# Optimization experiments

Hardware: AMD Instinct MI355X
Metric: run time of the kernel (lower is better)

Reference implementation:

```python
import jax, jax.numpy as jnp
import numpy as np

B, S, D_IN, E, H = 4, 2048, 768, 768, 12
HD = E // H                      # 64
WIN_PCT = 10                     # window_size init arg (percent of valid length)
MAX_LEN = 2048
MIN_WIN = 2
PAD = -1e9
TEMP = 1.0


def setup_inputs() -> dict:
    key = jax.random.key(0)
    k1, k2, k3 = jax.random.split(key, 3)
    return {
        "x": jax.random.normal(k1, (B, S, D_IN), dtype=jnp.float32),
        "src_key_padding_mask": jnp.zeros((B, S), dtype=jnp.int32),   # 0 = valid token
        "matrix_mask": jnp.zeros((B, S, S), dtype=jnp.float32),       # additive mask, 0 or PAD
        "qkv_w": jax.random.normal(k2, (3 * E, D_IN), dtype=jnp.float32) * 0.02,
        "qkv_b": jnp.zeros((3 * E,), dtype=jnp.float32),
        "o_w": jax.random.normal(k3, (E, E), dtype=jnp.float32) * 0.02,
        "o_b": jnp.zeros((E,), dtype=jnp.float32),
    }


def _sliding_window_mask(src_key_padding_mask, matrix_mask):
    # per-sample window size = ceil(valid_len * WIN_PCT / 100), clamped to >= MIN_WIN
    lens = (src_key_padding_mask == 0).sum(axis=1)                    # [B]
    clipped = jnp.minimum(lens, MAX_LEN).astype(jnp.float32)
    wsz = jnp.maximum(jnp.ceil(clipped * WIN_PCT / 100.0), MIN_WIN)   # [B] float ok for compare
    idx = jnp.arange(S)
    dist = jnp.abs(idx[None, :, None] - idx[None, None, :])           # [1,S,S]
    window_mask = dist > wsz[:, None, None]                           # [B,S,S] bool
    merged = window_mask | (matrix_mask == PAD)
    return jnp.where(merged, PAD, matrix_mask)                        # [B,S,S]


def reference(x, src_key_padding_mask, matrix_mask, qkv_w, qkv_b, o_w, o_b):
    mask = _sliding_window_mask(src_key_padding_mask, matrix_mask)    # [B,S,S]
    qkv = x @ qkv_w.T + qkv_b                                         # [B,S,3E]
    # torch: reshape(B,S,H,3*HD) then chunk along last dim
    qkv = qkv.reshape(B, S, H, 3 * HD).transpose(0, 2, 1, 3)          # [B,H,S,3*HD]
    q, k, v = jnp.split(qkv, 3, axis=-1)                              # each [B,H,S,HD]
    scale = 1.0 / np.sqrt(HD)
    logits = jnp.einsum("bhqd,bhkd->bhqk", q, k) * scale + mask[:, None]
    attn = jax.nn.softmax(logits / TEMP, axis=-1)                     # [B,H,S,S]
    values = jnp.einsum("bhqk,bhkd->bhqd", attn, v)                   # [B,H,S,HD]
    attn_mean = attn.mean(axis=1)                                     # [B,S,S]
    values = values.transpose(0, 2, 1, 3).reshape(B, S, E)            # [B,S,E]
    o = values @ o_w.T + o_b
    return (o, attn_mean)
```

## Files before the change

kernel.cpp:

```cpp
#include <hip/hip_runtime.h>

#define SEQ 2048
#define NB 4
#define DIN 768
#define EDIM 768
#define NH 12
#define QKVN 2304
#define QKW 1536
#define SCALE 0.125f
#define PADV -1e9f
#define INV12 (0.0833333333f)
#define PSW 520

typedef unsigned short ushort_t;
typedef __attribute__((ext_vector_type(8))) short bf16x8;
typedef __attribute__((ext_vector_type(4))) float f32x4;

__device__ __forceinline__ float bf2f(ushort_t u) {
    union { unsigned int i; float f; } v; v.i = ((unsigned int)u) << 16; return v.f;
}
__device__ __forceinline__ ushort_t f2bf(float f) {
    union { float f; unsigned int i; } v; v.f = f;
    unsigned int r = (v.i + 0x7fffu + ((v.i >> 16) & 1u)) >> 16;
    return (ushort_t)r;
}
__device__ __forceinline__ void gl_lds16(const ushort_t* g, ushort_t* l) {
    __builtin_amdgcn_global_load_lds(
        (const __attribute__((address_space(1))) unsigned int*)(g),
        (__attribute__((address_space(3))) unsigned int*)(l),
        16, 0, 0);
}

__global__ void wsz_kernel(const int* __restrict__ mask, int* __restrict__ wszp) {
    int b = blockIdx.x;
    __shared__ int cnt;
    if (threadIdx.x == 0) cnt = 0;
    __syncthreads();
    int local = 0;
    for (int s = threadIdx.x; s < SEQ; s += blockDim.x)
        local += (mask[b * SEQ + s] == 0) ? 1 : 0;
    for (int o = 32; o; o >>= 1) local += __shfl_down(local, o, 64);
    if ((threadIdx.x & 63) == 0) atomicAdd(&cnt, local);
    __syncthreads();
    if (threadIdx.x == 0) {
        int len = cnt; if (len > 2048) len = 2048;
        float w = ceilf(((float)len * 10.0f) / 100.0f);
        int wsz = (int)w;
        if (wsz < 2) wsz = 2;
        wszp[b] = wsz;
    }
}

__global__ void cvt_kernel(const float* __restrict__ in, ushort_t* __restrict__ out, int n4) {
    int i = blockIdx.x * blockDim.x + threadIdx.x;
    if (i < n4) {
        float4 f = ((const float4*)in)[i];
        ushort4 u;
        u.x = f2bf(f.x); u.y = f2bf(f.y); u.z = f2bf(f.z); u.w = f2bf(f.w);
        ((ushort4*)out)[i] = u;
    }
}

__global__ void flag_kernel(const float* __restrict__ mmask, const int* __restrict__ wszp,
                            int* __restrict__ flags) {
    const int b = blockIdx.z, i16 = blockIdx.y;
    const int wsz = wszp[b];
    const int i0 = i16 * 16;
    const int jt0 = max(0, i0 - wsz) >> 6;
    const int jt1 = min(SEQ - 1, i0 + 15 + wsz) >> 6;
    const int jt = jt0 + blockIdx.x;
    if (jt > jt1) return;
    int any = 0;
    for (int e = threadIdx.x; e < 1024; e += 256) {
        int row = e >> 6, col = e & 63;
        float v = mmask[((size_t)b * SEQ + i0 + row) * SEQ + jt * 64 + col];
        any |= (v != 0.f);
    }
    if (any) flags[(b * 128 + i16) * 32 + jt] = 1;
}

template<int MODE>
__global__ __launch_bounds__(256) void mfma_gemm128(
    const ushort_t* __restrict__ A, const ushort_t* __restrict__ Bw,
    const float* __restrict__ bias, float* __restrict__ outf,
    ushort_t* __restrict__ qk, ushort_t* __restrict__ vt, int N, int K)
{
    __shared__ __align__(16) ushort_t Al[128 * 64];
    __shared__ __align__(16) ushort_t Bl[128 * 64];
    const int tid  = threadIdx.x;
    const int w    = tid >> 6;
    const int l    = tid & 63;
    const int quad = l >> 4;
    const int lr   = l & 15;
    const int mw   = (w >> 1) * 64;
    const int nw   = (w & 1) * 64;
    const int bm   = blockIdx.y * 128;
    const int bn   = blockIdx.x * 128;
    const int srow = l >> 3;
    const int sg   = (l & 7) ^ srow;

    f32x4 acc[4][4];
    #pragma unroll
    for (int i = 0; i < 4; ++i)
        #pragma unroll
        for (int j = 0; j < 4; ++j)
            #pragma unroll
            for (int r = 0; r < 4; ++r) acc[i][j][r] = 0.f;

    const ushort_t* ga = A  + (size_t)(bm + w * 32 + srow) * K + sg * 8;
    const ushort_t* gb = Bw + (size_t)(bn + w * 32 + srow) * K + sg * 8;
    ushort_t* la = &Al[(w * 32) * 64];
    ushort_t* lb = &Bl[(w * 32) * 64];

    for (int k0 = 0; k0 < K; k0 += 64) {
        __syncthreads();
        #pragma unroll
        for (int i = 0; i < 4; ++i)
            gl_lds16(ga + (size_t)(i * 8) * K + k0, la + i * 8 * 64);
        #pragma unroll
        for (int i = 0; i < 4; ++i)
            gl_lds16(gb + (size_t)(i * 8) * K + k0, lb + i * 8 * 64);
        __syncthreads();
        #pragma unroll
        for (int s = 0; s < 2; ++s) {
            bf16x8 af[4], bf[4];
            #pragma unroll
            for (int t = 0; t < 4; ++t)
                af[t] = *(const bf16x8*)&Al[(mw + t * 16 + lr) * 64 + (((4 * s + quad) ^ (lr & 7)) * 8)];
            #pragma unroll
            for (int t = 0; t < 4; ++t)
                bf[t] = *(const bf16x8*)&Bl[(nw + t * 16 + lr) * 64 + (((4 * s + quad) ^ (lr & 7)) * 8)];
            #pragma unroll
            for (int mt = 0; mt < 4; ++mt)
                #pragma unroll
                for (int nt = 0; nt < 4; ++nt)
                    acc[mt][nt] = __builtin_amdgcn_mfma_f32_16x16x32_bf16(af[mt], bf[nt], acc[mt][nt], 0, 0, 0);
        }
    }

    #pragma unroll
    for (int nt = 0; nt < 4; ++nt) {
        const int gn = bn + nw + nt * 16 + lr;
        const float bv = bias[gn];
        const int hh  = gn / 192;
        const int rem = gn - hh * 192;
        #pragma unroll
        for (int mt = 0; mt < 4; ++mt) {
            const int gm0 = bm + mw + mt * 16 + quad * 4;
            if (MODE == 0) {
                #pragma unroll
                for (int r = 0; r < 4; ++r)
                    outf[(size_t)(gm0 + r) * N + gn] = acc[mt][nt][r] + bv;
            } else if (rem < 128) {
                #pragma unroll
                for (int r = 0; r < 4; ++r)
                    qk[(size_t)(gm0 + r) * QKW + hh * 128 + rem] = f2bf(acc[mt][nt][r] + bv);
            } else {
                const int bb  = gm0 >> 11;
                const int tok = gm0 & (SEQ - 1);
                ushort4 st;
                st.x = f2bf(acc[mt][nt][0] + bv);
                st.y = f2bf(acc[mt][nt][1] + bv);
                st.z = f2bf(acc[mt][nt][2] + bv);
                st.w = f2bf(acc[mt][nt][3] + bv);
                *(ushort4*)&vt[((size_t)(bb * NH + hh) * 64 + (rem - 128)) * SEQ + tok] = st;
            }
        }
    }
}

__global__ __launch_bounds__(512) void attn_kernel(
    const ushort_t* __restrict__ qk,
    const ushort_t* __restrict__ vt,
    const float* __restrict__ mmask,
    const int* __restrict__ wszp,
    const int* __restrict__ flags,
    ushort_t* __restrict__ values,
    float* __restrict__ attn_out)
{
    __shared__ __align__(16) ushort_t Ps[2][16 * PSW];
    __shared__ float lsump[2][4][16];
    const int tid  = threadIdx.x;
    const int w    = tid >> 6;
    const int hg   = w >> 2;
    const int ww   = w & 3;
    const int lane = tid & 63;
    const int quad = lane >> 4;
    const int lr   = lane & 15;

    const int lin  = blockIdx.x;
    const int s    = lin & 1;
    const int b    = (lin >> 1) & 3;
    const int i16  = (lin >> 3) + 64 * s;
    const int iq0  = i16 * 16;

    const int wsz  = wszp[b];
    const int jlo  = max(0, iq0 - wsz);
    const int jhi  = min(SEQ - 1, iq0 + 15 + wsz);
    const int jt0  = jlo >> 6;
    const int nch  = (jhi >> 6) - jt0 + 1;
    const int jbase = jt0 << 6;
    const int span  = nch << 6;
    const int fbase = (b * 128 + i16) * 32;

    const int arow = tid & 15;
    const int acg  = tid >> 4;
    float acc[16];
    #pragma unroll
    for (int k = 0; k < 16; ++k) acc[k] = 0.f;

    const ushort_t* kbase = qk + (size_t)b * SEQ * QKW + 64;
    const ushort_t* vhead = vt + (size_t)b * NH * 64 * SEQ;

    for (int hp = 0; hp < NH / 2; ++hp) {
        const int h  = hp * 2 + hg;
        const int hq = h * 128;
        const ushort_t* qbase = qk + (size_t)(b * SEQ + iq0 + lr) * QKW + hq;
        const bf16x8 qf0 = *(const bf16x8*)(qbase + quad * 8);
        const bf16x8 qf1 = *(const bf16x8*)(qbase + 32 + quad * 8);

        float ls[4] = {0.f, 0.f, 0.f, 0.f};
        #pragma unroll
        for (int cc = 0; cc < 2; ++cc) {
            const int ci = ww + cc * 4;
            if (ci < nch) {
                const int jc = jbase + ci * 64;
                f32x4 s4[4];
                #pragma unroll
                for (int t = 0; t < 4; ++t) {
                    const ushort_t* kr = kbase + (size_t)(jc + t * 16 + lr) * QKW + hq;
                    bf16x8 kf0 = *(const bf16x8*)(kr + quad * 8);
                    bf16x8 kf1 = *(const bf16x8*)(kr + 32 + quad * 8);
                    #pragma unroll
                    for (int r = 0; r < 4; ++r) s4[t][r] = 0.f;
                    s4[t] = __builtin_amdgcn_mfma_f32_16x16x32_bf16(qf0, kf0, s4[t], 0, 0, 0);
                    s4[t] = __builtin_amdgcn_mfma_f32_16x16x32_bf16(qf1, kf1, s4[t], 0, 0, 0);
                }
                const int anym = flags[fbase + jt0 + ci];
                #pragma unroll
                for (int t = 0; t < 4; ++t) {
                    const int gj = jc + t * 16 + lr;
                    #pragma unroll
                    for (int r = 0; r < 4; ++r) {
                        const int gi = iq0 + quad * 4 + r;
                        float mm = 0.f;
                        if (anym) mm = mmask[((size_t)b * SEQ + gi) * SEQ + gj];
                        const int dist = gi > gj ? gi - gj : gj - gi;
                        const float p = (dist > wsz) ? 0.f : __expf(fmaf(s4[t][r], SCALE, mm));
                        ls[r] += p;
                        Ps[hg][(quad * 4 + r) * PSW + (ci * 64 + t * 16 + lr)] = f2bf(p);
                    }
                }
            }
        }
        #pragma unroll
        for (int r = 0; r < 4; ++r) {
            #pragma unroll
            for (int m = 8; m; m >>= 1) ls[r] += __shfl_xor(ls[r], m, 16);
        }
        if (lr == 0) {
            #pragma unroll
            for (int r = 0; r < 4; ++r) lsump[hg][ww][quad * 4 + r] = ls[r];
        }
        __syncthreads();

        if (acg * 16 < span) {
            const float l0 = lsump[0][0][arow] + lsump[0][1][arow] + lsump[0][2][arow] + lsump[0][3][arow];
            const float l1 = lsump[1][0][arow] + lsump[1][1][arow] + lsump[1][2][arow] + lsump[1][3][arow];
            const float sc0 = INV12 / l0;
            const float sc1 = INV12 / l1;
            const ushort_t* p0 = &Ps[0][arow * PSW + acg * 16];
            const ushort_t* p1 = &Ps[1][arow * PSW + acg * 16];
            #pragma unroll
            for (int k = 0; k < 4; ++k) {
                ushort4 u0 = *(const ushort4*)(p0 + k * 4);
                ushort4 u1 = *(const ushort4*)(p1 + k * 4);
                acc[k * 4 + 0] = fmaf(bf2f(u0.x), sc0, fmaf(bf2f(u1.x), sc1, acc[k * 4 + 0]));
                acc[k * 4 + 1] = fmaf(bf2f(u0.y), sc0, fmaf(bf2f(u1.y), sc1, acc[k * 4 + 1]));
                acc[k * 4 + 2] = fmaf(bf2f(u0.z), sc0, fmaf(bf2f(u1.z), sc1, acc[k * 4 + 2]));
                acc[k * 4 + 3] = fmaf(bf2f(u0.w), sc0, fmaf(bf2f(u1.w), sc1, acc[k * 4 + 3]));
            }
        }

        {
            f32x4 oacc;
            #pragma unroll
            for (int r = 0; r < 4; ++r) oacc[r] = 0.f;
            const ushort_t* vrow = vhead + (size_t)(hq / 2 + ww * 16 + lr) * SEQ + jbase;
            for (int ci = 0; ci < nch; ++ci) {
                const int tok0 = ci * 64;
                #pragma unroll
                for (int s2 = 0; s2 < 2; ++s2) {
                    bf16x8 pa = *(const bf16x8*)&Ps[hg][lr * PSW + tok0 + s2 * 32 + quad * 8];
                    bf16x8 vf = *(const bf16x8*)(vrow + tok0 + s2 * 32 + quad * 8);
                    oacc = __builtin_amdgcn_mfma_f32_16x16x32_bf16(pa, vf, oacc, 0, 0, 0);
                }
            }
            float lr4[4];
            #pragma unroll
            for (int r = 0; r < 4; ++r)
                lr4[r] = lsump[hg][0][quad * 4 + r] + lsump[hg][1][quad * 4 + r] +
                         lsump[hg][2][quad * 4 + r] + lsump[hg][3][quad * 4 + r];
            #pragma unroll
            for (int r = 0; r < 4; ++r) {
                const int row = iq0 + quad * 4 + r;
                values[(size_t)(b * SEQ + row) * EDIM + h * 64 + ww * 16 + lr] =
                    f2bf(oacc[r] / lr4[r]);
            }
        }
        __syncthreads();
    }

    if (acg * 16 < span) {
        float* dst = attn_out + ((size_t)b * SEQ + iq0 + arow) * SEQ + jbase + acg * 16;
        #pragma unroll
        for (int k = 0; k < 4; ++k) {
            float4 v = { acc[k * 4 + 0], acc[k * 4 + 1], acc[k * 4 + 2], acc[k * 4 + 3] };
            *(float4*)(dst + k * 4) = v;
        }
    }
    {
        const int c4lo = jbase >> 2;
        const int c4hi = (jbase + span) >> 2;
        const float4 z = {0.f, 0.f, 0.f, 0.f};
        for (int f = tid; f < 16 * 512; f += 512) {
            const int i  = f >> 9;
            const int c4 = f & 511;
            if (c4 < c4lo || c4 >= c4hi)
                *(float4*)(attn_out + ((size_t)b * SEQ + iq0 + i) * SEQ + c4 * 4) = z;
        }
    }
}

extern "C" void kernel_launch(void* const* d_in, const int* in_sizes, int n_in,
                              void* d_out, int out_size, void* d_ws, size_t ws_size,
                              hipStream_t stream) {
    const float* x      = (const float*)d_in[0];
    const int*   pad    = (const int*)d_in[1];
    const float* mmask  = (const float*)d_in[2];
    const float* qkv_w  = (const float*)d_in[3];
    const float* qkv_b  = (const float*)d_in[4];
    const float* o_w    = (const float*)d_in[5];
    const float* o_b    = (const float*)d_in[6];

    float* out_o    = (float*)d_out;
    float* out_attn = out_o + (size_t)NB * SEQ * EDIM;

    ushort_t* qk     = (ushort_t*)d_ws;
    ushort_t* vt     = qk + (size_t)NB * SEQ * QKW;
    ushort_t* xb     = vt + (size_t)NB * NH * 64 * SEQ;
    ushort_t* values = xb;
    ushort_t* wqkvb  = xb + (size_t)NB * SEQ * DIN;
    ushort_t* wob    = wqkvb + (size_t)QKVN * DIN;
    int*      wszp   = (int*)(wob + (size_t)EDIM * EDIM);
    int*      flags  = wszp + 4;

    hipMemsetAsync(flags, 0, (size_t)NB * 128 * 32 * sizeof(int), stream);

    wsz_kernel<<<NB, 256, 0, stream>>>(pad, wszp);
    flag_kernel<<<dim3(8, 128, NB), 256, 0, stream>>>(mmask, wszp, flags);

    const int nx = NB * SEQ * DIN / 4, nw1 = QKVN * DIN / 4, nw2 = EDIM * EDIM / 4;
    cvt_kernel<<<(nx  + 255) / 256, 256, 0, stream>>>(x,     xb,    nx);
    cvt_kernel<<<(nw1 + 255) / 256, 256, 0, stream>>>(qkv_w, wqkvb, nw1);
    cvt_kernel<<<(nw2 + 255) / 256, 256, 0, stream>>>(o_w,   wob,   nw2);

    mfma_gemm128<1><<<dim3(QKVN / 128, (NB * SEQ) / 128), 256, 0, stream>>>(
        xb, wqkvb, qkv_b, nullptr, qk, vt, QKVN, DIN);

    attn_kernel<<<512, 512, 0, stream>>>(
        qk, vt, mmask, wszp, flags, values, out_attn);

    mfma_gemm128<0><<<dim3(EDIM / 128, (NB * SEQ) / 128), 256, 0, stream>>>(
        values, wob, o_b, out_o, nullptr, nullptr, EDIM, EDIM);
}
```

Baseline: 345.1 us.

## Halve attention query tile to 8 rows, double blocks; merge convert kernels

The attention kernel now processes 8 query rows per block instead of 16 and launches 1024 blocks instead of 512. The 16-row MFMA tiles are filled by duplicating the 8 query rows, and only the valid half is stored. This raises block-level parallelism and shrinks the key span each block covers, at the cost of half-wasted MFMA work and duplicated K/V loads. The three fp32-to-bf16 convert launches are also merged into a single kernel to cut launch overhead.

```diff
diff --git a/kernel.cpp b/kernel.cpp
--- a/kernel.cpp
+++ b/kernel.cpp
@@ -11,6 +11,7 @@
 #define PADV -1e9f
 #define INV12 (0.0833333333f)
 #define PSW 520
+#define TQR 8
 
 typedef unsigned short ushort_t;
 typedef __attribute__((ext_vector_type(8))) short bf16x8;
@@ -51,14 +52,21 @@
     }
 }
 
-__global__ void cvt_kernel(const float* __restrict__ in, ushort_t* __restrict__ out, int n4) {
+__global__ void cvt3_kernel(const float* __restrict__ s0, int n0,
+                            const float* __restrict__ s1, int n1,
+                            const float* __restrict__ s2, int n2,
+                            ushort_t* __restrict__ d0, ushort_t* __restrict__ d1,
+                            ushort_t* __restrict__ d2) {
     int i = blockIdx.x * blockDim.x + threadIdx.x;
-    if (i < n4) {
-        float4 f = ((const float4*)in)[i];
-        ushort4 u;
-        u.x = f2bf(f.x); u.y = f2bf(f.y); u.z = f2bf(f.z); u.w = f2bf(f.w);
-        ((ushort4*)out)[i] = u;
-    }
+    const float* src; ushort_t* dst; int off;
+    if (i < n0)               { src = s0; dst = d0; off = i; }
+    else if (i < n0 + n1)     { src = s1; dst = d1; off = i - n0; }
+    else if (i < n0 + n1 + n2){ src = s2; dst = d2; off = i - n0 - n1; }
+    else return;
+    float4 f = ((const float4*)src)[off];
+    ushort4 u;
+    u.x = f2bf(f.x); u.y = f2bf(f.y); u.z = f2bf(f.z); u.w = f2bf(f.w);
+    ((ushort4*)dst)[off] = u;
 }
 
 __global__ void flag_kernel(const float* __restrict__ mmask, const int* __restrict__ wszp,
@@ -178,8 +186,8 @@
     ushort_t* __restrict__ values,
     float* __restrict__ attn_out)
 {
-    __shared__ __align__(16) ushort_t Ps[2][16 * PSW];
-    __shared__ float lsump[2][4][16];
+    __shared__ __align__(16) ushort_t Ps[2][TQR * PSW];
+    __shared__ float lsump[2][4][TQR];
     const int tid  = threadIdx.x;
     const int w    = tid >> 6;
     const int hg   = w >> 2;
@@ -191,31 +199,32 @@
     const int lin  = blockIdx.x;
     const int s    = lin & 1;
     const int b    = (lin >> 1) & 3;
-    const int i16  = (lin >> 3) + 64 * s;
-    const int iq0  = i16 * 16;
+    const int i8   = (lin >> 3) + 128 * s;
+    const int iq0  = i8 * TQR;
 
     const int wsz  = wszp[b];
     const int jlo  = max(0, iq0 - wsz);
-    const int jhi  = min(SEQ - 1, iq0 + 15 + wsz);
+    const int jhi  = min(SEQ - 1, iq0 + TQR - 1 + wsz);
     const int jt0  = jlo >> 6;
     const int nch  = (jhi >> 6) - jt0 + 1;
     const int jbase = jt0 << 6;
     const int span  = nch << 6;
-    const int fbase = (b * 128 + i16) * 32;
-
-    const int arow = tid & 15;
-    const int acg  = tid >> 4;
-    float acc[16];
+    const int fbase = (b * 128 + (i8 >> 1)) * 32;
+
+    const int arow = tid & 7;
+    const int acg  = tid >> 3;
+    float acc[8];
     #pragma unroll
-    for (int k = 0; k < 16; ++k) acc[k] = 0.f;
+    for (int k = 0; k < 8; ++k) acc[k] = 0.f;
 
     const ushort_t* kbase = qk + (size_t)b * SEQ * QKW + 64;
     const ushort_t* vhead = vt + (size_t)b * NH * 64 * SEQ;
+    const int qrow = iq0 + (lr & 7);
 
     for (int hp = 0; hp < NH / 2; ++hp) {
         const int h  = hp * 2 + hg;
         const int hq = h * 128;
-        const ushort_t* qbase = qk + (size_t)(b * SEQ + iq0 + lr) * QKW + hq;
+        const ushort_t* qbase = qk + (size_t)(b * SEQ + qrow) * QKW + hq;
         const bf16x8 qf0 = *(const bf16x8*)(qbase + quad * 8);
         const bf16x8 qf1 = *(const bf16x8*)(qbase + 32 + quad * 8);
 
@@ -242,13 +251,15 @@
                     const int gj = jc + t * 16 + lr;
                     #pragma unroll
                     for (int r = 0; r < 4; ++r) {
-                        const int gi = iq0 + quad * 4 + r;
+                        const int rloc = quad * 4 + r;
+                        const int gi = iq0 + (rloc & 7);
                         float mm = 0.f;
                         if (anym) mm = mmask[((size_t)b * SEQ + gi) * SEQ + gj];
                         const int dist = gi > gj ? gi - gj : gj - gi;
                         const float p = (dist > wsz) ? 0.f : __expf(fmaf(s4[t][r], SCALE, mm));
                         ls[r] += p;
-                        Ps[hg][(quad * 4 + r) * PSW + (ci * 64 + t * 16 + lr)] = f2bf(p);
+                        if (rloc < TQR)
+                            Ps[hg][rloc * PSW + (ci * 64 + t * 16 + lr)] = f2bf(p);
                     }
                 }
             }
@@ -258,21 +269,21 @@
             #pragma unroll
             for (int m = 8; m; m >>= 1) ls[r] += __shfl_xor(ls[r], m, 16);
         }
-        if (lr == 0) {
+        if (lr == 0 && quad < 2) {
             #pragma unroll
             for (int r = 0; r < 4; ++r) lsump[hg][ww][quad * 4 + r] = ls[r];
         }
         __syncthreads();
 
-        if (acg * 16 < span) {
+        if (acg * 8 < span) {
             const float l0 = lsump[0][0][arow] + lsump[0][1][arow] + lsump[0][2][arow] + lsump[0][3][arow];
             const float l1 = lsump[1][0][arow] + lsump[1][1][arow] + lsump[1][2][arow] + lsump[1][3][arow];
             const float sc0 = INV12 / l0;
             const float sc1 = INV12 / l1;
-            const ushort_t* p0 = &Ps[0][arow * PSW + acg * 16];
-            const ushort_t* p1 = &Ps[1][arow * PSW + acg * 16];
-            #pragma unroll
-            for (int k = 0; k < 4; ++k) {
+            const ushort_t* p0 = &Ps[0][arow * PSW + acg * 8];
+            const ushort_t* p1 = &Ps[1][arow * PSW + acg * 8];
+            #pragma unroll
+            for (int k = 0; k < 2; ++k) {
                 ushort4 u0 = *(const ushort4*)(p0 + k * 4);
                 ushort4 u1 = *(const ushort4*)(p1 + k * 4);
                 acc[k * 4 + 0] = fmaf(bf2f(u0.x), sc0, fmaf(bf2f(u1.x), sc1, acc[k * 4 + 0]));
@@ -286,35 +297,38 @@
             f32x4 oacc;
             #pragma unroll
             for (int r = 0; r < 4; ++r) oacc[r] = 0.f;
-            const ushort_t* vrow = vhead + (size_t)(hq / 2 + ww * 16 + lr) * SEQ + jbase;
+            const ushort_t* vrow = vhead + (size_t)(h * 64 + ww * 16 + lr) * SEQ + jbase;
+            const ushort_t* prow = &Ps[hg][(lr & 7) * PSW];
             for (int ci = 0; ci < nch; ++ci) {
                 const int tok0 = ci * 64;
                 #pragma unroll
                 for (int s2 = 0; s2 < 2; ++s2) {
-                    bf16x8 pa = *(const bf16x8*)&Ps[hg][lr * PSW + tok0 + s2 * 32 + quad * 8];
+                    bf16x8 pa = *(const bf16x8*)(prow + tok0 + s2 * 32 + quad * 8);
                     bf16x8 vf = *(const bf16x8*)(vrow + tok0 + s2 * 32 + quad * 8);
                     oacc = __builtin_amdgcn_mfma_f32_16x16x32_bf16(pa, vf, oacc, 0, 0, 0);
                 }
             }
-            float lr4[4];
-            #pragma unroll
-            for (int r = 0; r < 4; ++r)
-                lr4[r] = lsump[hg][0][quad * 4 + r] + lsump[hg][1][quad * 4 + r] +
-                         lsump[hg][2][quad * 4 + r] + lsump[hg][3][quad * 4 + r];
-            #pragma unroll
-            for (int r = 0; r < 4; ++r) {
-                const int row = iq0 + quad * 4 + r;
-                values[(size_t)(b * SEQ + row) * EDIM + h * 64 + ww * 16 + lr] =
-                    f2bf(oacc[r] / lr4[r]);
+            if (quad < 2) {
+                float lr4[4];
+                #pragma unroll
+                for (int r = 0; r < 4; ++r)
+                    lr4[r] = lsump[hg][0][quad * 4 + r] + lsump[hg][1][quad * 4 + r] +
+                             lsump[hg][2][quad * 4 + r] + lsump[hg][3][quad * 4 + r];
+                #pragma unroll
+                for (int r = 0; r < 4; ++r) {
+                    const int row = iq0 + quad * 4 + r;
+                    values[(size_t)(b * SEQ + row) * EDIM + h * 64 + ww * 16 + lr] =
+                        f2bf(oacc[r] / lr4[r]);
+                }
             }
         }
         __syncthreads();
     }
 
-    if (acg * 16 < span) {
-        float* dst = attn_out + ((size_t)b * SEQ + iq0 + arow) * SEQ + jbase + acg * 16;
-        #pragma unroll
-        for (int k = 0; k < 4; ++k) {
+    if (acg * 8 < span) {
+        float* dst = attn_out + ((size_t)b * SEQ + iq0 + arow) * SEQ + jbase + acg * 8;
+        #pragma unroll
+        for (int k = 0; k < 2; ++k) {
             float4 v = { acc[k * 4 + 0], acc[k * 4 + 1], acc[k * 4 + 2], acc[k * 4 + 3] };
             *(float4*)(dst + k * 4) = v;
         }
@@ -323,7 +337,7 @@
         const int c4lo = jbase >> 2;
         const int c4hi = (jbase + span) >> 2;
         const float4 z = {0.f, 0.f, 0.f, 0.f};
-        for (int f = tid; f < 16 * 512; f += 512) {
+        for (int f = tid; f < TQR * 512; f += 512) {
             const int i  = f >> 9;
             const int c4 = f & 511;
             if (c4 < c4lo || c4 >= c4hi)
@@ -361,14 +375,13 @@
     flag_kernel<<<dim3(8, 128, NB), 256, 0, stream>>>(mmask, wszp, flags);
 
     const int nx = NB * SEQ * DIN / 4, nw1 = QKVN * DIN / 4, nw2 = EDIM * EDIM / 4;
-    cvt_kernel<<<(nx  + 255) / 256, 256, 0, stream>>>(x,     xb,    nx);
-    cvt_kernel<<<(nw1 + 255) / 256, 256, 0, stream>>>(qkv_w, wqkvb, nw1);
-    cvt_kernel<<<(nw2 + 255) / 256, 256, 0, stream>>>(o_w,   wob,   nw2);
+    cvt3_kernel<<<(nx + nw1 + nw2 + 255) / 256, 256, 0, stream>>>(
+        x, nx, qkv_w, nw1, o_w, nw2, xb, wqkvb, wob);
 
     mfma_gemm128<1><<<dim3(QKVN / 128, (NB * SEQ) / 128), 256, 0, stream>>>(
         xb, wqkvb, qkv_b, nullptr, qk, vt, QKVN, DIN);
 
-    attn_kernel<<<512, 512, 0, stream>>>(
+    attn_kernel<<<1024, 512, 0, stream>>>(
         qk, vt, mmask, wszp, flags, values, out_attn);
 
     mfma_gemm128<0><<<dim3(EDIM / 128, (NB * SEQ) / 128), 256, 0, stream>>>(
```

Measured after the change: 472.2 us. 1.37x slower.

## Process three heads per attention iteration with 768-thread blocks; merge conversion kernels

Applied to the files above, without the earlier changes.

The attention kernel now runs 12 waves per block, so three heads are handled at once instead of two. This cuts the number of head iterations and block-wide barriers from six to four, and the per-row attention mean now sums three probability buffers per pass. The three fp32-to-bf16 conversion launches are folded into one kernel that picks its source by index, which saves launch overhead. In exchange the block uses more shared memory and has more threads competing for registers, which could lower occupancy.

```diff
diff --git a/kernel.cpp b/kernel.cpp
--- a/kernel.cpp
+++ b/kernel.cpp
@@ -51,14 +51,21 @@
     }
 }
 
-__global__ void cvt_kernel(const float* __restrict__ in, ushort_t* __restrict__ out, int n4) {
+__global__ void cvt3_kernel(const float* __restrict__ s0, int n0,
+                            const float* __restrict__ s1, int n1,
+                            const float* __restrict__ s2, int n2,
+                            ushort_t* __restrict__ d0, ushort_t* __restrict__ d1,
+                            ushort_t* __restrict__ d2) {
     int i = blockIdx.x * blockDim.x + threadIdx.x;
-    if (i < n4) {
-        float4 f = ((const float4*)in)[i];
-        ushort4 u;
-        u.x = f2bf(f.x); u.y = f2bf(f.y); u.z = f2bf(f.z); u.w = f2bf(f.w);
-        ((ushort4*)out)[i] = u;
-    }
+    const float* src; ushort_t* dst; int off;
+    if (i < n0)               { src = s0; dst = d0; off = i; }
+    else if (i < n0 + n1)     { src = s1; dst = d1; off = i - n0; }
+    else if (i < n0 + n1 + n2){ src = s2; dst = d2; off = i - n0 - n1; }
+    else return;
+    float4 f = ((const float4*)src)[off];
+    ushort4 u;
+    u.x = f2bf(f.x); u.y = f2bf(f.y); u.z = f2bf(f.z); u.w = f2bf(f.w);
+    ((ushort4*)dst)[off] = u;
 }
 
 __global__ void flag_kernel(const float* __restrict__ mmask, const int* __restrict__ wszp,
@@ -169,7 +176,7 @@
     }
 }
 
-__global__ __launch_bounds__(512) void attn_kernel(
+__global__ __launch_bounds__(768) void attn_kernel(
     const ushort_t* __restrict__ qk,
     const ushort_t* __restrict__ vt,
     const float* __restrict__ mmask,
@@ -178,8 +185,8 @@
     ushort_t* __restrict__ values,
     float* __restrict__ attn_out)
 {
-    __shared__ __align__(16) ushort_t Ps[2][16 * PSW];
-    __shared__ float lsump[2][4][16];
+    __shared__ __align__(16) ushort_t Ps[3][16 * PSW];
+    __shared__ float lsump[3][4][16];
     const int tid  = threadIdx.x;
     const int w    = tid >> 6;
     const int hg   = w >> 2;
@@ -212,8 +219,8 @@
     const ushort_t* kbase = qk + (size_t)b * SEQ * QKW + 64;
     const ushort_t* vhead = vt + (size_t)b * NH * 64 * SEQ;
 
-    for (int hp = 0; hp < NH / 2; ++hp) {
-        const int h  = hp * 2 + hg;
+    for (int hp = 0; hp < NH / 3; ++hp) {
+        const int h  = hp * 3 + hg;
         const int hq = h * 128;
         const ushort_t* qbase = qk + (size_t)(b * SEQ + iq0 + lr) * QKW + hq;
         const bf16x8 qf0 = *(const bf16x8*)(qbase + quad * 8);
@@ -264,21 +271,25 @@
         }
         __syncthreads();
 
-        if (acg * 16 < span) {
+        if (acg < 32 && acg * 16 < span) {
             const float l0 = lsump[0][0][arow] + lsump[0][1][arow] + lsump[0][2][arow] + lsump[0][3][arow];
             const float l1 = lsump[1][0][arow] + lsump[1][1][arow] + lsump[1][2][arow] + lsump[1][3][arow];
+            const float l2 = lsump[2][0][arow] + lsump[2][1][arow] + lsump[2][2][arow] + lsump[2][3][arow];
             const float sc0 = INV12 / l0;
             const float sc1 = INV12 / l1;
+            const float sc2 = INV12 / l2;
             const ushort_t* p0 = &Ps[0][arow * PSW + acg * 16];
             const ushort_t* p1 = &Ps[1][arow * PSW + acg * 16];
+            const ushort_t* p2 = &Ps[2][arow * PSW + acg * 16];
             #pragma unroll
             for (int k = 0; k < 4; ++k) {
                 ushort4 u0 = *(const ushort4*)(p0 + k * 4);
                 ushort4 u1 = *(const ushort4*)(p1 + k * 4);
-                acc[k * 4 + 0] = fmaf(bf2f(u0.x), sc0, fmaf(bf2f(u1.x), sc1, acc[k * 4 + 0]));
-                acc[k * 4 + 1] = fmaf(bf2f(u0.y), sc0, fmaf(bf2f(u1.y), sc1, acc[k * 4 + 1]));
-                acc[k * 4 + 2] = fmaf(bf2f(u0.z), sc0, fmaf(bf2f(u1.z), sc1, acc[k * 4 + 2]));
-                acc[k * 4 + 3] = fmaf(bf2f(u0.w), sc0, fmaf(bf2f(u1.w), sc1, acc[k * 4 + 3]));
+                ushort4 u2 = *(const ushort4*)(p2 + k * 4);
+                acc[k * 4 + 0] += bf2f(u0.x) * sc0 + bf2f(u1.x) * sc1 + bf2f(u2.x) * sc2;
+                acc[k * 4 + 1] += bf2f(u0.y) * sc0 + bf2f(u1.y) * sc1 + bf2f(u2.y) * sc2;
+                acc[k * 4 + 2] += bf2f(u0.z) * sc0 + bf2f(u1.z) * sc1 + bf2f(u2.z) * sc2;
+                acc[k * 4 + 3] += bf2f(u0.w) * sc0 + bf2f(u1.w) * sc1 + bf2f(u2.w) * sc2;
             }
         }
 
@@ -286,7 +297,7 @@
             f32x4 oacc;
             #pragma unroll
             for (int r = 0; r < 4; ++r) oacc[r] = 0.f;
-            const ushort_t* vrow = vhead + (size_t)(hq / 2 + ww * 16 + lr) * SEQ + jbase;
+            const ushort_t* vrow = vhead + (size_t)(h * 64 + ww * 16 + lr) * SEQ + jbase;
             for (int ci = 0; ci < nch; ++ci) {
                 const int tok0 = ci * 64;
                 #pragma unroll
@@ -311,7 +322,7 @@
         __syncthreads();
     }
 
-    if (acg * 16 < span) {
+    if (acg < 32 && acg * 16 < span) {
         float* dst = attn_out + ((size_t)b * SEQ + iq0 + arow) * SEQ + jbase + acg * 16;
         #pragma unroll
         for (int k = 0; k < 4; ++k) {
@@ -323,7 +334,7 @@
         const int c4lo = jbase >> 2;
         const int c4hi = (jbase + span) >> 2;
         const float4 z = {0.f, 0.f, 0.f, 0.f};
-        for (int f = tid; f < 16 * 512; f += 512) {
+        for (int f = tid; f < 16 * 512; f += 768) {
             const int i  = f >> 9;
             const int c4 = f & 511;
             if (c4 < c4lo || c4 >= c4hi)
@@ -361,14 +372,13 @@
     flag_kernel<<<dim3(8, 128, NB), 256, 0, stream>>>(mmask, wszp, flags);
 
     const int nx = NB * SEQ * DIN / 4, nw1 = QKVN * DIN / 4, nw2 = EDIM * EDIM / 4;
-    cvt_kernel<<<(nx  + 255) / 256, 256, 0, stream>>>(x,     xb,    nx);
-    cvt_kernel<<<(nw1 + 255) / 256, 256, 0, stream>>>(qkv_w, wqkvb, nw1);
-    cvt_kernel<<<(nw2 + 255) / 256, 256, 0, stream>>>(o_w,   wob,   nw2);
+    cvt3_kernel<<<(nx + nw1 + nw2 + 255) / 256, 256, 0, stream>>>(
+        x, nx, qkv_w, nw1, o_w, nw2, xb, wqkvb, wob);
 
     mfma_gemm128<1><<<dim3(QKVN / 128, (NB * SEQ) / 128), 256, 0, stream>>>(
         xb, wqkvb, qkv_b, nullptr, qk, vt, QKVN, DIN);
 
-    attn_kernel<<<512, 512, 0, stream>>>(
+    attn_kernel<<<512, 768, 0, stream>>>(
         qk, vt, mmask, wszp, flags, values, out_attn);
 
     mfma_gemm128<0><<<dim3(EDIM / 128, (NB * SEQ) / 128), 256, 0, stream>>>(
```

Result: no change. 344.4 us (-0.2%).

## Fuse window-size and mask-flag computation into attention, merge conversions, head-major QK

Applied to the files above, without the earlier changes.

Removes the separate window-size kernel, the flag kernel and the memset. Each attention block now computes the valid length and the per-chunk nonzero-mask flags itself in shared memory. The three fp32-to-bf16 conversion launches are merged into one, and the Q/K projection output is stored head-major ([B,H,S,128]) so K rows for a head are contiguous. This cuts launch overhead and may improve locality of K loads. In exchange, every attention block redundantly reads the padding mask and its mask tiles.

```diff
diff --git a/kernel.cpp b/kernel.cpp
--- a/kernel.cpp
+++ b/kernel.cpp
@@ -6,7 +6,6 @@
 #define EDIM 768
 #define NH 12
 #define QKVN 2304
-#define QKW 1536
 #define SCALE 0.125f
 #define PADV -1e9f
 #define INV12 (0.0833333333f)
@@ -31,59 +30,28 @@
         16, 0, 0);
 }
 
-__global__ void wsz_kernel(const int* __restrict__ mask, int* __restrict__ wszp) {
-    int b = blockIdx.x;
-    __shared__ int cnt;
-    if (threadIdx.x == 0) cnt = 0;
-    __syncthreads();
-    int local = 0;
-    for (int s = threadIdx.x; s < SEQ; s += blockDim.x)
-        local += (mask[b * SEQ + s] == 0) ? 1 : 0;
-    for (int o = 32; o; o >>= 1) local += __shfl_down(local, o, 64);
-    if ((threadIdx.x & 63) == 0) atomicAdd(&cnt, local);
-    __syncthreads();
-    if (threadIdx.x == 0) {
-        int len = cnt; if (len > 2048) len = 2048;
-        float w = ceilf(((float)len * 10.0f) / 100.0f);
-        int wsz = (int)w;
-        if (wsz < 2) wsz = 2;
-        wszp[b] = wsz;
-    }
-}
-
-__global__ void cvt_kernel(const float* __restrict__ in, ushort_t* __restrict__ out, int n4) {
+__global__ void cvt3_kernel(const float* __restrict__ s0, int n0,
+                            const float* __restrict__ s1, int n1,
+                            const float* __restrict__ s2, int n2,
+                            ushort_t* __restrict__ d0, ushort_t* __restrict__ d1,
+                            ushort_t* __restrict__ d2) {
     int i = blockIdx.x * blockDim.x + threadIdx.x;
-    if (i < n4) {
-        float4 f = ((const float4*)in)[i];
-        ushort4 u;
-        u.x = f2bf(f.x); u.y = f2bf(f.y); u.z = f2bf(f.z); u.w = f2bf(f.w);
-        ((ushort4*)out)[i] = u;
-    }
-}
-
-__global__ void flag_kernel(const float* __restrict__ mmask, const int* __restrict__ wszp,
-                            int* __restrict__ flags) {
-    const int b = blockIdx.z, i16 = blockIdx.y;
-    const int wsz = wszp[b];
-    const int i0 = i16 * 16;
-    const int jt0 = max(0, i0 - wsz) >> 6;
-    const int jt1 = min(SEQ - 1, i0 + 15 + wsz) >> 6;
-    const int jt = jt0 + blockIdx.x;
-    if (jt > jt1) return;
-    int any = 0;
-    for (int e = threadIdx.x; e < 1024; e += 256) {
-        int row = e >> 6, col = e & 63;
-        float v = mmask[((size_t)b * SEQ + i0 + row) * SEQ + jt * 64 + col];
-        any |= (v != 0.f);
-    }
-    if (any) flags[(b * 128 + i16) * 32 + jt] = 1;
+    const float* src; ushort_t* dst; int off;
+    if (i < n0)               { src = s0; dst = d0; off = i; }
+    else if (i < n0 + n1)     { src = s1; dst = d1; off = i - n0; }
+    else if (i < n0 + n1 + n2){ src = s2; dst = d2; off = i - n0 - n1; }
+    else return;
+    float4 f = ((const float4*)src)[off];
+    ushort4 u;
+    u.x = f2bf(f.x); u.y = f2bf(f.y); u.z = f2bf(f.z); u.w = f2bf(f.w);
+    ((ushort4*)dst)[off] = u;
 }
 
 template<int MODE>
 __global__ __launch_bounds__(256) void mfma_gemm128(
     const ushort_t* __restrict__ A, const ushort_t* __restrict__ Bw,
     const float* __restrict__ bias, float* __restrict__ outf,
-    ushort_t* __restrict__ qk, ushort_t* __restrict__ vt, int N, int K)
+    ushort_t* __restrict__ qkh, ushort_t* __restrict__ vt, int N, int K)
 {
     __shared__ __align__(16) ushort_t Al[128 * 64];
     __shared__ __align__(16) ushort_t Bl[128 * 64];
@@ -152,9 +120,12 @@
                 for (int r = 0; r < 4; ++r)
                     outf[(size_t)(gm0 + r) * N + gn] = acc[mt][nt][r] + bv;
             } else if (rem < 128) {
+                const int bb  = gm0 >> 11;
+                const int tok = gm0 & (SEQ - 1);
                 #pragma unroll
                 for (int r = 0; r < 4; ++r)
-                    qk[(size_t)(gm0 + r) * QKW + hh * 128 + rem] = f2bf(acc[mt][nt][r] + bv);
+                    qkh[((size_t)(bb * NH + hh) * SEQ + tok + r) * 128 + rem] =
+                        f2bf(acc[mt][nt][r] + bv);
             } else {
                 const int bb  = gm0 >> 11;
                 const int tok = gm0 & (SEQ - 1);
@@ -170,16 +141,17 @@
 }
 
 __global__ __launch_bounds__(512) void attn_kernel(
-    const ushort_t* __restrict__ qk,
+    const ushort_t* __restrict__ qkh,
     const ushort_t* __restrict__ vt,
     const float* __restrict__ mmask,
-    const int* __restrict__ wszp,
-    const int* __restrict__ flags,
+    const int* __restrict__ pad,
     ushort_t* __restrict__ values,
     float* __restrict__ attn_out)
 {
     __shared__ __align__(16) ushort_t Ps[2][16 * PSW];
     __shared__ float lsump[2][4][16];
+    __shared__ int s_cnt[8];
+    __shared__ int s_flags[8];
     const int tid  = threadIdx.x;
     const int w    = tid >> 6;
     const int hg   = w >> 2;
@@ -194,28 +166,53 @@
     const int i16  = (lin >> 3) + 64 * s;
     const int iq0  = i16 * 16;
 
-    const int wsz  = wszp[b];
+    {
+        int4 pv = *(const int4*)&pad[b * SEQ + tid * 4];
+        int c = (pv.x == 0) + (pv.y == 0) + (pv.z == 0) + (pv.w == 0);
+        #pragma unroll
+        for (int o = 32; o; o >>= 1) c += __shfl_down(c, o, 64);
+        if (lane == 0) s_cnt[w] = c;
+        if (tid < 8) s_flags[tid] = 0;
+    }
+    __syncthreads();
+    int len = 0;
+    #pragma unroll
+    for (int k = 0; k < 8; ++k) len += s_cnt[k];
+    if (len > 2048) len = 2048;
+    int wsz = (int)ceilf((float)len * 10.0f / 100.0f);
+    if (wsz < 2) wsz = 2;
+
     const int jlo  = max(0, iq0 - wsz);
     const int jhi  = min(SEQ - 1, iq0 + 15 + wsz);
     const int jt0  = jlo >> 6;
     const int nch  = (jhi >> 6) - jt0 + 1;
     const int jbase = jt0 << 6;
     const int span  = nch << 6;
-    const int fbase = (b * 128 + i16) * 32;
+
+    {
+        const float* tp = mmask + ((size_t)b * SEQ + iq0) * SEQ + jbase;
+        const int e = tid * 2, row = e >> 6, col = e & 63;
+        for (int ci = 0; ci < nch; ++ci) {
+            float2 v = *(const float2*)&tp[(size_t)row * SEQ + ci * 64 + col];
+            if (__any(v.x != 0.f || v.y != 0.f)) {
+                if (lane == 0) atomicOr(&s_flags[ci], 1);
+            }
+        }
+    }
 
     const int arow = tid & 15;
     const int acg  = tid >> 4;
     float acc[16];
     #pragma unroll
     for (int k = 0; k < 16; ++k) acc[k] = 0.f;
-
-    const ushort_t* kbase = qk + (size_t)b * SEQ * QKW + 64;
+    __syncthreads();
+
     const ushort_t* vhead = vt + (size_t)b * NH * 64 * SEQ;
 
     for (int hp = 0; hp < NH / 2; ++hp) {
-        const int h  = hp * 2 + hg;
-        const int hq = h * 128;
-        const ushort_t* qbase = qk + (size_t)(b * SEQ + iq0 + lr) * QKW + hq;
+        const int h = hp * 2 + hg;
+        const ushort_t* hbase = qkh + (size_t)(b * NH + h) * SEQ * 128;
+        const ushort_t* qbase = hbase + (size_t)(iq0 + lr) * 128;
         const bf16x8 qf0 = *(const bf16x8*)(qbase + quad * 8);
         const bf16x8 qf1 = *(const bf16x8*)(qbase + 32 + quad * 8);
 
@@ -228,7 +225,7 @@
                 f32x4 s4[4];
                 #pragma unroll
                 for (int t = 0; t < 4; ++t) {
-                    const ushort_t* kr = kbase + (size_t)(jc + t * 16 + lr) * QKW + hq;
+                    const ushort_t* kr = hbase + (size_t)(jc + t * 16 + lr) * 128 + 64;
                     bf16x8 kf0 = *(const bf16x8*)(kr + quad * 8);
                     bf16x8 kf1 = *(const bf16x8*)(kr + 32 + quad * 8);
                     #pragma unroll
@@ -236,7 +233,7 @@
                     s4[t] = __builtin_amdgcn_mfma_f32_16x16x32_bf16(qf0, kf0, s4[t], 0, 0, 0);
                     s4[t] = __builtin_amdgcn_mfma_f32_16x16x32_bf16(qf1, kf1, s4[t], 0, 0, 0);
                 }
-                const int anym = flags[fbase + jt0 + ci];
+                const int anym = s_flags[ci];
                 #pragma unroll
                 for (int t = 0; t < 4; ++t) {
                     const int gj = jc + t * 16 + lr;
@@ -286,7 +283,7 @@
             f32x4 oacc;
             #pragma unroll
             for (int r = 0; r < 4; ++r) oacc[r] = 0.f;
-            const ushort_t* vrow = vhead + (size_t)(hq / 2 + ww * 16 + lr) * SEQ + jbase;
+            const ushort_t* vrow = vhead + (size_t)(h * 64 + ww * 16 + lr) * SEQ + jbase;
             for (int ci = 0; ci < nch; ++ci) {
                 const int tok0 = ci * 64;
                 #pragma unroll
@@ -346,30 +343,22 @@
     float* out_o    = (float*)d_out;
     float* out_attn = out_o + (size_t)NB * SEQ * EDIM;
 
-    ushort_t* qk     = (ushort_t*)d_ws;
-    ushort_t* vt     = qk + (size_t)NB * SEQ * QKW;
+    ushort_t* qkh    = (ushort_t*)d_ws;
+    ushort_t* vt     = qkh + (size_t)NB * NH * SEQ * 128;
     ushort_t* xb     = vt + (size_t)NB * NH * 64 * SEQ;
     ushort_t* values = xb;
     ushort_t* wqkvb  = xb + (size_t)NB * SEQ * DIN;
     ushort_t* wob    = wqkvb + (size_t)QKVN * DIN;
-    int*      wszp   = (int*)(wob + (size_t)EDIM * EDIM);
-    int*      flags  = wszp + 4;
-
-    hipMemsetAsync(flags, 0, (size_t)NB * 128 * 32 * sizeof(int), stream);
-
-    wsz_kernel<<<NB, 256, 0, stream>>>(pad, wszp);
-    flag_kernel<<<dim3(8, 128, NB), 256, 0, stream>>>(mmask, wszp, flags);
 
     const int nx = NB * SEQ * DIN / 4, nw1 = QKVN * DIN / 4, nw2 = EDIM * EDIM / 4;
-    cvt_kernel<<<(nx  + 255) / 256, 256, 0, stream>>>(x,     xb,    nx);
-    cvt_kernel<<<(nw1 + 255) / 256, 256, 0, stream>>>(qkv_w, wqkvb, nw1);
-    cvt_kernel<<<(nw2 + 255) / 256, 256, 0, stream>>>(o_w,   wob,   nw2);
+    cvt3_kernel<<<(nx + nw1 + nw2 + 255) / 256, 256, 0, stream>>>(
+        x, nx, qkv_w, nw1, o_w, nw2, xb, wqkvb, wob);
 
     mfma_gemm128<1><<<dim3(QKVN / 128, (NB * SEQ) / 128), 256, 0, stream>>>(
-        xb, wqkvb, qkv_b, nullptr, qk, vt, QKVN, DIN);
+        xb, wqkvb, qkv_b, nullptr, qkh, vt, QKVN, DIN);
 
     attn_kernel<<<512, 512, 0, stream>>>(
-        qk, vt, mmask, wszp, flags, values, out_attn);
+        qkh, vt, mmask, pad, values, out_attn);
 
     mfma_gemm128<0><<<dim3(EDIM / 128, (NB * SEQ) / 128), 256, 0, stream>>>(
         values, wob, o_b, out_o, nullptr, nullptr, EDIM, EDIM);
```

After: 328.9 us. 1.05x faster.
